# Kernel tuning notes

Measured on AMD Instinct MI355X. Metric: run time of the kernel, lower is better.

Reference implementation:

```python
import jax, jax.numpy as jnp
import numpy as np

CH = 128
GROUPS = 8
EPS = 1e-5


def setup_inputs() -> dict:
    key = jax.random.key(0)
    ks = jax.random.split(key, 12)
    b, c, h, w = 16, CH, 64, 64
    x = jax.random.normal(ks[0], (b, c, h, w), dtype=jnp.float32)
    s = 1.0 / np.sqrt(c)
    return {
        "x": x,
        "gn_w": jnp.ones((c,), jnp.float32),
        "gn_b": jnp.zeros((c,), jnp.float32),
        "wq": jax.random.normal(ks[1], (c, c), jnp.float32) * s,
        "bq": jax.random.normal(ks[2], (c,), jnp.float32) * 0.01,
        "wk": jax.random.normal(ks[3], (c, c), jnp.float32) * s,
        "bk": jax.random.normal(ks[4], (c,), jnp.float32) * 0.01,
        "wv": jax.random.normal(ks[5], (c, c), jnp.float32) * s,
        "bv": jax.random.normal(ks[6], (c,), jnp.float32) * 0.01,
        "wf": jax.random.normal(ks[7], (c, c), jnp.float32) * s,
        "bf": jax.random.normal(ks[8], (c,), jnp.float32) * 0.01,
    }


def _group_norm(x, gamma, beta):
    b, c, h, w = x.shape
    xg = x.reshape(b, GROUPS, -1)  # [b, g, (c/g)*h*w]
    mean = xg.mean(axis=-1, keepdims=True)
    var = xg.var(axis=-1, keepdims=True)
    xn = ((xg - mean) * jax.lax.rsqrt(var + EPS)).reshape(b, c, h, w)
    return xn * gamma[None, :, None, None] + beta[None, :, None, None]


def reference(x, gn_w, gn_b, wq, bq, wk, bk, wv, bv, wf, bf):
    b, c, h, w = x.shape
    x_gn = _group_norm(x, gn_w, gn_b)
    xf = x_gn.reshape(b, c, h * w)  # [b, c, n]
    # 1x1 convs == per-position channel matmuls
    q = jnp.einsum('oc,bcn->bon', wq, xf) + bq[None, :, None]
    k = jnp.einsum('oc,bcn->bon', wk, xf) + bk[None, :, None]
    v = jnp.einsum('oc,bcn->bon', wv, xf) + bv[None, :, None]
    scale = c ** (-0.5)
    attn = jnp.einsum('bci,bcj->bij', q, k) * scale  # [b, n, n]
    attn = jax.nn.softmax(attn, axis=-1)
    # out[b,c,i] = sum_j v[b,c,j] * attn[b,i,j]
    o = jnp.einsum('bcj,bij->bci', v, attn)
    of = jnp.einsum('oc,bcn->bon', wf, o) + bf[None, :, None]
    return of.reshape(b, c, h, w) + x
```

## Files before the change

### kernel.cpp

```cpp
#include <hip/hip_runtime.h>

#define NB   16
#define NC   128
#define NPOS 4096

typedef short bf16x8 __attribute__((ext_vector_type(8)));
typedef float f32x4  __attribute__((ext_vector_type(4)));
typedef float f32x16 __attribute__((ext_vector_type(16)));

static __device__ __forceinline__ unsigned short f2bf(float f) {
    unsigned int u = __builtin_bit_cast(unsigned int, f);
    u += 0x7FFFu + ((u >> 16) & 1u);
    return (unsigned short)(u >> 16);
}

static __device__ __forceinline__ unsigned int pkbf(float hi, float lo) {
    return __builtin_amdgcn_perm(__builtin_bit_cast(unsigned int, hi),
                                 __builtin_bit_cast(unsigned int, lo), 0x07060302u);
}

__global__ void wconv_kernel(const float* __restrict__ wq, const float* __restrict__ wk,
                             const float* __restrict__ wv, const float* __restrict__ wf,
                             unsigned short* __restrict__ oq, unsigned short* __restrict__ ok,
                             unsigned short* __restrict__ ov, unsigned short* __restrict__ of) {
    int i = blockIdx.x * 256 + threadIdx.x;
    oq[i] = f2bf(wq[i]); ok[i] = f2bf(wk[i]); ov[i] = f2bf(wv[i]); of[i] = f2bf(wf[i]);
}

__global__ void gnstat_kernel(const float* __restrict__ x, float* __restrict__ mean,
                              float* __restrict__ rstd) {
    int bg = blockIdx.x;
    const float* p = x + (size_t)bg * 65536;
    int t = threadIdx.x;
    float s = 0.f, q = 0.f;
    for (int it = 0; it < 64; ++it) {
        f32x4 v = *(const f32x4*)(p + it * 1024 + t * 4);
        s += v[0] + v[1] + v[2] + v[3];
        q += v[0] * v[0] + v[1] * v[1] + v[2] * v[2] + v[3] * v[3];
    }
    for (int m = 1; m < 64; m <<= 1) { s += __shfl_xor(s, m); q += __shfl_xor(q, m); }
    __shared__ float ls[4], lq[4];
    int w = t >> 6;
    if ((t & 63) == 0) { ls[w] = s; lq[w] = q; }
    __syncthreads();
    if (t == 0) {
        s = ls[0] + ls[1] + ls[2] + ls[3];
        q = lq[0] + lq[1] + lq[2] + lq[3];
        float mu  = s * (1.0f / 65536.0f);
        float var = q * (1.0f / 65536.0f) - mu * mu;
        mean[bg] = mu;
        rstd[bg] = rsqrtf(var + 1e-5f);
    }
}

__global__ __launch_bounds__(256) void qkv_kernel(
    const float* __restrict__ x, const float* __restrict__ gnw, const float* __restrict__ gnb,
    const float* __restrict__ mean, const float* __restrict__ rstd,
    const unsigned short* __restrict__ wqb, const unsigned short* __restrict__ wkb,
    const unsigned short* __restrict__ wvb,
    const float* __restrict__ bq, const float* __restrict__ bk, const float* __restrict__ bv,
    unsigned short* __restrict__ qT, unsigned short* __restrict__ kT, unsigned short* __restrict__ vv) {
    __shared__ __attribute__((aligned(16))) unsigned short xn[64 * 136];
    const int b = blockIdx.y, i0 = blockIdx.x * 64;
    const int t = threadIdx.x;
    {
        int iL = (t & 15) * 4;
        int cb = (t >> 4) * 2;
        for (int cg = 0; cg < 4; ++cg) {
            int c = cg * 32 + cb;
            int g = c >> 4;
            float mu = mean[b * 8 + g], rs = rstd[b * 8 + g];
            float ga0 = gnw[c] * rs,     be0 = gnb[c]     - mu * ga0;
            float ga1 = gnw[c + 1] * rs, be1 = gnb[c + 1] - mu * ga1;
            const float* p0 = x + ((size_t)(b * NC + c)) * NPOS + i0 + iL;
            f32x4 v0 = *(const f32x4*)p0;
            f32x4 v1 = *(const f32x4*)(p0 + NPOS);
            for (int e = 0; e < 4; ++e) {
                unsigned int u = (unsigned)f2bf(v0[e] * ga0 + be0) |
                                 ((unsigned)f2bf(v1[e] * ga1 + be1) << 16);
                *(unsigned int*)&xn[(iL + e) * 136 + c] = u;
            }
        }
    }
    __syncthreads();

    const int lane = t & 63, w = t >> 6, quad = lane >> 4, li = lane & 15;

    bf16x8 ax[4];
    for (int kc = 0; kc < 4; ++kc)
        ax[kc] = *(const bf16x8*)&xn[(w * 16 + li) * 136 + kc * 32 + quad * 8];
    for (int wt = 0; wt < 2; ++wt) {
        const unsigned short* W = wt ? wkb : wqb;
        const float* bias = wt ? bk : bq;
        unsigned short* dst = wt ? kT : qT;
        for (int nt = 0; nt < 8; ++nt) {
            f32x4 d = {0.f, 0.f, 0.f, 0.f};
            for (int kc = 0; kc < 4; ++kc) {
                bf16x8 bw = *(const bf16x8*)&W[(nt * 16 + li) * 128 + kc * 32 + quad * 8];
                d = __builtin_amdgcn_mfma_f32_16x16x32_bf16(ax[kc], bw, d, 0, 0, 0);
            }
            float bb = bias[nt * 16 + li];
            size_t base = ((size_t)b * NPOS + i0 + w * 16 + quad * 4) * NC + nt * 16 + li;
            for (int rr = 0; rr < 4; ++rr)
                dst[base + (size_t)rr * NC] = f2bf(d[rr] + bb);
        }
    }

    bf16x8 av[2][4];
    for (int mt = 0; mt < 2; ++mt)
        for (int kc = 0; kc < 4; ++kc)
            av[mt][kc] = *(const bf16x8*)&wvb[((w * 2 + mt) * 16 + li) * 128 + kc * 32 + quad * 8];
    for (int nt = 0; nt < 4; ++nt) {
        bf16x8 bx[4];
        for (int kc = 0; kc < 4; ++kc)
            bx[kc] = *(const bf16x8*)&xn[(nt * 16 + li) * 136 + kc * 32 + quad * 8];
        for (int mt = 0; mt < 2; ++mt) {
            f32x4 d = {0.f, 0.f, 0.f, 0.f};
            for (int kc = 0; kc < 4; ++kc)
                d = __builtin_amdgcn_mfma_f32_16x16x32_bf16(av[mt][kc], bx[kc], d, 0, 0, 0);
            int o0 = (w * 2 + mt) * 16 + quad * 4;
            for (int rr = 0; rr < 4; ++rr) {
                float val = d[rr] + bv[o0 + rr];
                vv[((size_t)(b * NC + o0 + rr)) * NPOS + i0 + nt * 16 + li] = f2bf(val);
            }
        }
    }
}

__global__ __launch_bounds__(256, 2) void flash_kernel(
    const unsigned short* __restrict__ qT, const unsigned short* __restrict__ kT,
    const unsigned short* __restrict__ vv, unsigned short* __restrict__ oT) {
    __shared__ __attribute__((aligned(16))) unsigned short kt[64 * 128];
    __shared__ __attribute__((aligned(16))) unsigned short vt[128 * 64];
    __shared__ __attribute__((aligned(16))) unsigned short pt[4 * 2048];
    const int b = blockIdx.x, i0 = blockIdx.y * 128;
    const int t = threadIdx.x, lane = t & 63, w = t >> 6;
    const int il = lane & 31, h = lane >> 5;
    const float SC = 0.12751743075095855f;
    const float CP = 1.001953125f;

    bf16x8 qb[8];
    for (int kc = 0; kc < 8; ++kc)
        qb[kc] = *(const bf16x8*)&qT[((size_t)b * NPOS + i0 + w * 32 + il) * NC + kc * 16 + h * 8];

    float mrow = -1e30f, lrow = 0.f;
    f32x16 acc[4];
    for (int ct = 0; ct < 4; ++ct)
        for (int r = 0; r < 16; ++r) acc[ct][r] = 0.f;

    const int kjj = t >> 2, kq = t & 3;
    const int vc  = t >> 1, vq = t & 1;
    const unsigned short* pw = &pt[w * 2048];

    for (int jt = 0; jt < 64; ++jt) {
        const int j0 = jt * 64;
        __syncthreads();
        {
            const unsigned short* sk = &kT[((size_t)b * NPOS + j0 + kjj) * NC + kq * 32];
            unsigned short* dkb = &kt[kjj * 128];
            const unsigned short* sv = &vv[((size_t)(b * NC + vc)) * NPOS + j0 + vq * 32];
            unsigned short* dvb = &vt[vc * 64];
            for (int m = 0; m < 4; ++m) {
                *(bf16x8*)(dkb + (((kq * 4 + m) ^ (kjj & 7)) << 3)) = *(const bf16x8*)(sk + m * 8);
                *(bf16x8*)(dvb + (((vq * 4 + m) ^ (vc  & 7)) << 3)) = *(const bf16x8*)(sv + m * 8);
            }
        }
        __syncthreads();

        f32x16 st0, st1;
        for (int r = 0; r < 16; ++r) { st0[r] = 0.f; st1[r] = 0.f; }
        for (int kc = 0; kc < 8; ++kc) {
            bf16x8 a0 = *(const bf16x8*)&kt[il * 128 + (((kc * 2 + h) ^ (il & 7)) << 3)];
            bf16x8 a1 = *(const bf16x8*)&kt[(32 + il) * 128 + (((kc * 2 + h) ^ (il & 7)) << 3)];
            st0 = __builtin_amdgcn_mfma_f32_32x32x16_bf16(a0, qb[kc], st0, 0, 0, 0);
            st1 = __builtin_amdgcn_mfma_f32_32x32x16_bf16(a1, qb[kc], st1, 0, 0, 0);
        }

        float mx = st0[0];
        for (int r = 1; r < 16; ++r) mx = fmaxf(mx, st0[r]);
        for (int r = 0; r < 16; ++r) mx = fmaxf(mx, st1[r]);
        mx *= SC;
        mx = fmaxf(mx, __shfl_xor(mx, 32));
        float mn = fmaxf(mrow, mx);
        float alpha = __builtin_amdgcn_exp2f(mrow - mn);
        mrow = mn;

        float p0[16], p1[16], rs = 0.f;
        for (int r = 0; r < 16; ++r) {
            p0[r] = __builtin_amdgcn_exp2f(st0[r] * SC - mn);
            p1[r] = __builtin_amdgcn_exp2f(st1[r] * SC - mn);
            rs += p0[r] + p1[r];
        }
        rs += __shfl_xor(rs, 32);
        lrow = lrow * alpha + rs;

        for (int r2 = 0; r2 < 4; ++r2) {
            unsigned short* dp = (unsigned short*)&pw[il * 64 + 4 * h];
            unsigned int a0 = pkbf(p0[r2 * 4 + 1] * CP, p0[r2 * 4 + 0] * CP);
            unsigned int a1 = pkbf(p0[r2 * 4 + 3] * CP, p0[r2 * 4 + 2] * CP);
            unsigned int b0 = pkbf(p1[r2 * 4 + 1] * CP, p1[r2 * 4 + 0] * CP);
            unsigned int b1 = pkbf(p1[r2 * 4 + 3] * CP, p1[r2 * 4 + 2] * CP);
            *(unsigned int*)(dp + (((0 * 4 + r2) ^ (il & 7)) << 3))     = a0;
            *(unsigned int*)(dp + (((0 * 4 + r2) ^ (il & 7)) << 3) + 2) = a1;
            *(unsigned int*)(dp + (((1 * 4 + r2) ^ (il & 7)) << 3))     = b0;
            *(unsigned int*)(dp + (((1 * 4 + r2) ^ (il & 7)) << 3) + 2) = b1;
        }

        float alb[16];
        for (int r = 0; r < 16; ++r)
            alb[r] = __shfl(alpha, (r & 3) + 8 * (r >> 2) + 4 * h);
        for (int ct = 0; ct < 4; ++ct)
            for (int r = 0; r < 16; ++r) acc[ct][r] *= alb[r];

        bf16x8 ap[4];
        for (int kc2 = 0; kc2 < 4; ++kc2)
            ap[kc2] = *(const bf16x8*)&pw[il * 64 + (((kc2 * 2 + h) ^ (il & 7)) << 3)];
        for (int ct = 0; ct < 4; ++ct) {
            int cr = ct * 32 + il;
            for (int kc2 = 0; kc2 < 4; ++kc2) {
                bf16x8 bv = *(const bf16x8*)&vt[cr * 64 + (((kc2 * 2 + h) ^ (cr & 7)) << 3)];
                acc[ct] = __builtin_amdgcn_mfma_f32_32x32x16_bf16(ap[kc2], bv, acc[ct], 0, 0, 0);
            }
        }
    }

    float inv = __builtin_amdgcn_rcpf(lrow);
    float invb[16];
    for (int r = 0; r < 16; ++r)
        invb[r] = __shfl(inv, (r & 3) + 8 * (r >> 2) + 4 * h);
    for (int ct = 0; ct < 4; ++ct)
        for (int r = 0; r < 16; ++r) {
            int ir = (r & 3) + 8 * (r >> 2) + 4 * h;
            oT[((size_t)b * NPOS + i0 + w * 32 + ir) * NC + ct * 32 + il] =
                f2bf(acc[ct][r] * invb[r]);
        }
}

__global__ __launch_bounds__(256) void proj_kernel(
    const unsigned short* __restrict__ oT, const unsigned short* __restrict__ wfb,
    const float* __restrict__ bf_, const float* __restrict__ x, float* __restrict__ out) {
    const int b = blockIdx.y, i0 = blockIdx.x * 64;
    const int t = threadIdx.x, lane = t & 63, w = t >> 6, quad = lane >> 4, li = lane & 15;
    bf16x8 aw[2][4];
    for (int mt = 0; mt < 2; ++mt)
        for (int kc = 0; kc < 4; ++kc)
            aw[mt][kc] = *(const bf16x8*)&wfb[((w * 2 + mt) * 16 + li) * 128 + kc * 32 + quad * 8];
    for (int nt = 0; nt < 4; ++nt) {
        bf16x8 bo[4];
        for (int kc = 0; kc < 4; ++kc)
            bo[kc] = *(const bf16x8*)&oT[((size_t)b * NPOS + i0 + nt * 16 + li) * NC + kc * 32 + quad * 8];
        for (int mt = 0; mt < 2; ++mt) {
            f32x4 d = {0.f, 0.f, 0.f, 0.f};
            for (int kc = 0; kc < 4; ++kc)
                d = __builtin_amdgcn_mfma_f32_16x16x32_bf16(aw[mt][kc], bo[kc], d, 0, 0, 0);
            int o0 = (w * 2 + mt) * 16 + quad * 4;
            for (int rr = 0; rr < 4; ++rr) {
                size_t idx = ((size_t)(b * NC + o0 + rr)) * NPOS + i0 + nt * 16 + li;
                out[idx] = d[rr] + bf_[o0 + rr] + x[idx];
            }
        }
    }
}

extern "C" void kernel_launch(void* const* d_in, const int* in_sizes, int n_in,
                              void* d_out, int out_size, void* d_ws, size_t ws_size,
                              hipStream_t stream) {
    const float* x   = (const float*)d_in[0];
    const float* gnw = (const float*)d_in[1];
    const float* gnb = (const float*)d_in[2];
    const float* wq  = (const float*)d_in[3];
    const float* bq  = (const float*)d_in[4];
    const float* wk  = (const float*)d_in[5];
    const float* bk  = (const float*)d_in[6];
    const float* wv  = (const float*)d_in[7];
    const float* bv  = (const float*)d_in[8];
    const float* wf  = (const float*)d_in[9];
    const float* bf_ = (const float*)d_in[10];
    float* out = (float*)d_out;

    char* ws = (char*)d_ws;
    float* mean = (float*)(ws + 0);
    float* rstd = (float*)(ws + 512);
    unsigned short* wqb = (unsigned short*)(ws + 1024);
    unsigned short* wkb = wqb + 16384;
    unsigned short* wvb = wkb + 16384;
    unsigned short* wfb = wvb + 16384;
    unsigned short* qT  = (unsigned short*)(ws + 132096);
    unsigned short* kT  = qT + (size_t)NB * NPOS * NC;
    unsigned short* vv  = kT + (size_t)NB * NPOS * NC;
    unsigned short* oT  = vv + (size_t)NB * NPOS * NC;

    wconv_kernel<<<64, 256, 0, stream>>>(wq, wk, wv, wf, wqb, wkb, wvb, wfb);
    gnstat_kernel<<<128, 256, 0, stream>>>(x, mean, rstd);
    dim3 g(64, 16);
    qkv_kernel<<<g, 256, 0, stream>>>(x, gnw, gnb, mean, rstd, wqb, wkb, wvb, bq, bk, bv, qT, kT, vv);
    dim3 gf(16, 32);
    flash_kernel<<<gf, 256, 0, stream>>>(qT, kT, vv, oT);
    proj_kernel<<<g, 256, 0, stream>>>(oT, wfb, bf_, x, out);
}
```

Baseline: 352.3 us.

## Keep softmax P in registers via lane shuffles and fold scale into Q

The flash kernel now computes the PV product with V as the A operand and P as the B operand. The P fragments are built directly from the score accumulators with cross-half lane shuffles, which removes the per-wave shared-memory round trip for P and the per-row alpha/inv broadcasts. The softmax scale is folded into Q during the projection, and the bf16 rounding correction is moved into the exponent offset. Removing the P buffer frees shared memory, so the occupancy hint is raised to 3 blocks per SM; this may add register pressure or spills. Loops are unrolled, and the output is stored as packed pairs.

```diff
diff --git a/kernel.cpp b/kernel.cpp
--- a/kernel.cpp
+++ b/kernel.cpp
@@ -7,6 +7,9 @@
 typedef short bf16x8 __attribute__((ext_vector_type(8)));
 typedef float f32x4  __attribute__((ext_vector_type(4)));
 typedef float f32x16 __attribute__((ext_vector_type(16)));
+typedef unsigned int u32x4 __attribute__((ext_vector_type(4)));
+
+#define SCF 0.12751743075095855f
 
 static __device__ __forceinline__ unsigned short f2bf(float f) {
     unsigned int u = __builtin_bit_cast(unsigned int, f);
@@ -93,6 +96,7 @@
         const unsigned short* W = wt ? wkb : wqb;
         const float* bias = wt ? bk : bq;
         unsigned short* dst = wt ? kT : qT;
+        const float osc = wt ? 1.0f : SCF;
         for (int nt = 0; nt < 8; ++nt) {
             f32x4 d = {0.f, 0.f, 0.f, 0.f};
             for (int kc = 0; kc < 4; ++kc) {
@@ -102,7 +106,7 @@
             float bb = bias[nt * 16 + li];
             size_t base = ((size_t)b * NPOS + i0 + w * 16 + quad * 4) * NC + nt * 16 + li;
             for (int rr = 0; rr < 4; ++rr)
-                dst[base + (size_t)rr * NC] = f2bf(d[rr] + bb);
+                dst[base + (size_t)rr * NC] = f2bf((d[rr] + bb) * osc);
         }
     }
 
@@ -127,17 +131,14 @@
     }
 }
 
-__global__ __launch_bounds__(256, 2) void flash_kernel(
+__global__ __launch_bounds__(256, 3) void flash_kernel(
     const unsigned short* __restrict__ qT, const unsigned short* __restrict__ kT,
     const unsigned short* __restrict__ vv, unsigned short* __restrict__ oT) {
     __shared__ __attribute__((aligned(16))) unsigned short kt[64 * 128];
     __shared__ __attribute__((aligned(16))) unsigned short vt[128 * 64];
-    __shared__ __attribute__((aligned(16))) unsigned short pt[4 * 2048];
     const int b = blockIdx.x, i0 = blockIdx.y * 128;
     const int t = threadIdx.x, lane = t & 63, w = t >> 6;
     const int il = lane & 31, h = lane >> 5;
-    const float SC = 0.12751743075095855f;
-    const float CP = 1.001953125f;
 
     bf16x8 qb[8];
     for (int kc = 0; kc < 8; ++kc)
@@ -150,25 +151,25 @@
 
     const int kjj = t >> 2, kq = t & 3;
     const int vc  = t >> 1, vq = t & 1;
-    const unsigned short* pw = &pt[w * 2048];
+    const unsigned short* ksrc = &kT[((size_t)b * NPOS + kjj) * NC + kq * 32];
+    const unsigned short* vsrc = &vv[((size_t)(b * NC + vc)) * NPOS + vq * 32];
+    unsigned short* dkb = &kt[kjj * 128];
+    unsigned short* dvb = &vt[vc * 64];
 
     for (int jt = 0; jt < 64; ++jt) {
-        const int j0 = jt * 64;
         __syncthreads();
-        {
-            const unsigned short* sk = &kT[((size_t)b * NPOS + j0 + kjj) * NC + kq * 32];
-            unsigned short* dkb = &kt[kjj * 128];
-            const unsigned short* sv = &vv[((size_t)(b * NC + vc)) * NPOS + j0 + vq * 32];
-            unsigned short* dvb = &vt[vc * 64];
-            for (int m = 0; m < 4; ++m) {
-                *(bf16x8*)(dkb + (((kq * 4 + m) ^ (kjj & 7)) << 3)) = *(const bf16x8*)(sk + m * 8);
-                *(bf16x8*)(dvb + (((vq * 4 + m) ^ (vc  & 7)) << 3)) = *(const bf16x8*)(sv + m * 8);
-            }
-        }
+        #pragma unroll
+        for (int m = 0; m < 4; ++m) {
+            *(bf16x8*)(dkb + (((kq * 4 + m) ^ (kjj & 7)) << 3)) = *(const bf16x8*)(ksrc + m * 8);
+            *(bf16x8*)(dvb + (((vq * 4 + m) ^ (vc  & 7)) << 3)) = *(const bf16x8*)(vsrc + m * 8);
+        }
+        ksrc += 64 * NC;
+        vsrc += 64;
         __syncthreads();
 
         f32x16 st0, st1;
         for (int r = 0; r < 16; ++r) { st0[r] = 0.f; st1[r] = 0.f; }
+        #pragma unroll
         for (int kc = 0; kc < 8; ++kc) {
             bf16x8 a0 = *(const bf16x8*)&kt[il * 128 + (((kc * 2 + h) ^ (il & 7)) << 3)];
             bf16x8 a1 = *(const bf16x8*)&kt[(32 + il) * 128 + (((kc * 2 + h) ^ (il & 7)) << 3)];
@@ -177,62 +178,70 @@
         }
 
         float mx = st0[0];
+        #pragma unroll
         for (int r = 1; r < 16; ++r) mx = fmaxf(mx, st0[r]);
+        #pragma unroll
         for (int r = 0; r < 16; ++r) mx = fmaxf(mx, st1[r]);
-        mx *= SC;
         mx = fmaxf(mx, __shfl_xor(mx, 32));
         float mn = fmaxf(mrow, mx);
         float alpha = __builtin_amdgcn_exp2f(mrow - mn);
         mrow = mn;
-
-        float p0[16], p1[16], rs = 0.f;
+        float mc = mn - 0.0028150156f;
+
+        float p0[16], p1[16];
+        float rs = 0.f;
+        #pragma unroll
         for (int r = 0; r < 16; ++r) {
-            p0[r] = __builtin_amdgcn_exp2f(st0[r] * SC - mn);
-            p1[r] = __builtin_amdgcn_exp2f(st1[r] * SC - mn);
+            p0[r] = __builtin_amdgcn_exp2f(st0[r] - mc);
+            p1[r] = __builtin_amdgcn_exp2f(st1[r] - mc);
             rs += p0[r] + p1[r];
         }
         rs += __shfl_xor(rs, 32);
         lrow = lrow * alpha + rs;
 
-        for (int r2 = 0; r2 < 4; ++r2) {
-            unsigned short* dp = (unsigned short*)&pw[il * 64 + 4 * h];
-            unsigned int a0 = pkbf(p0[r2 * 4 + 1] * CP, p0[r2 * 4 + 0] * CP);
-            unsigned int a1 = pkbf(p0[r2 * 4 + 3] * CP, p0[r2 * 4 + 2] * CP);
-            unsigned int b0 = pkbf(p1[r2 * 4 + 1] * CP, p1[r2 * 4 + 0] * CP);
-            unsigned int b1 = pkbf(p1[r2 * 4 + 3] * CP, p1[r2 * 4 + 2] * CP);
-            *(unsigned int*)(dp + (((0 * 4 + r2) ^ (il & 7)) << 3))     = a0;
-            *(unsigned int*)(dp + (((0 * 4 + r2) ^ (il & 7)) << 3) + 2) = a1;
-            *(unsigned int*)(dp + (((1 * 4 + r2) ^ (il & 7)) << 3))     = b0;
-            *(unsigned int*)(dp + (((1 * 4 + r2) ^ (il & 7)) << 3) + 2) = b1;
-        }
-
-        float alb[16];
-        for (int r = 0; r < 16; ++r)
-            alb[r] = __shfl(alpha, (r & 3) + 8 * (r >> 2) + 4 * h);
+        bf16x8 pfrag[4];
+        #pragma unroll
+        for (int hf = 0; hf < 2; ++hf) {
+            const float* pp = hf ? p1 : p0;
+            #pragma unroll
+            for (int c2 = 0; c2 < 2; ++c2) {
+                int rb = c2 * 8;
+                unsigned int A0 = pkbf(pp[rb + 1], pp[rb + 0]);
+                unsigned int A1 = pkbf(pp[rb + 3], pp[rb + 2]);
+                unsigned int B0 = pkbf(pp[rb + 5], pp[rb + 4]);
+                unsigned int B1 = pkbf(pp[rb + 7], pp[rb + 6]);
+                unsigned int s0 = h ? A0 : B0, s1 = h ? A1 : B1;
+                unsigned int r0 = __shfl_xor(s0, 32), r1 = __shfl_xor(s1, 32);
+                u32x4 f;
+                f[0] = h ? r0 : A0; f[1] = h ? r1 : A1;
+                f[2] = h ? B0 : r0; f[3] = h ? B1 : r1;
+                pfrag[hf * 2 + c2] = __builtin_bit_cast(bf16x8, f);
+            }
+        }
+
+        #pragma unroll
         for (int ct = 0; ct < 4; ++ct)
-            for (int r = 0; r < 16; ++r) acc[ct][r] *= alb[r];
-
-        bf16x8 ap[4];
-        for (int kc2 = 0; kc2 < 4; ++kc2)
-            ap[kc2] = *(const bf16x8*)&pw[il * 64 + (((kc2 * 2 + h) ^ (il & 7)) << 3)];
+            #pragma unroll
+            for (int r = 0; r < 16; ++r) acc[ct][r] *= alpha;
+        #pragma unroll
         for (int ct = 0; ct < 4; ++ct) {
             int cr = ct * 32 + il;
+            #pragma unroll
             for (int kc2 = 0; kc2 < 4; ++kc2) {
-                bf16x8 bv = *(const bf16x8*)&vt[cr * 64 + (((kc2 * 2 + h) ^ (cr & 7)) << 3)];
-                acc[ct] = __builtin_amdgcn_mfma_f32_32x32x16_bf16(ap[kc2], bv, acc[ct], 0, 0, 0);
+                bf16x8 av = *(const bf16x8*)&vt[cr * 64 + (((kc2 * 2 + h) ^ (cr & 7)) << 3)];
+                acc[ct] = __builtin_amdgcn_mfma_f32_32x32x16_bf16(av, pfrag[kc2], acc[ct], 0, 0, 0);
             }
         }
     }
 
     float inv = __builtin_amdgcn_rcpf(lrow);
-    float invb[16];
-    for (int r = 0; r < 16; ++r)
-        invb[r] = __shfl(inv, (r & 3) + 8 * (r >> 2) + 4 * h);
+    unsigned short* orow = &oT[((size_t)b * NPOS + i0 + w * 32 + il) * NC];
+    #pragma unroll
     for (int ct = 0; ct < 4; ++ct)
-        for (int r = 0; r < 16; ++r) {
-            int ir = (r & 3) + 8 * (r >> 2) + 4 * h;
-            oT[((size_t)b * NPOS + i0 + w * 32 + ir) * NC + ct * 32 + il] =
-                f2bf(acc[ct][r] * invb[r]);
+        #pragma unroll
+        for (int r = 0; r < 16; r += 2) {
+            int c = ct * 32 + (r & 3) + 8 * (r >> 2) + 4 * h;
+            *(unsigned int*)&orow[c] = pkbf(acc[ct][r + 1] * inv, acc[ct][r] * inv);
         }
 }
 
```

New measurement: 369.2 us. 4.8% more time.
